# Kernel optimization log

Hardware: AMD Instinct MI355X
Metric: run time of the kernel (lower is better)

Reference implementation:

```python
import jax, jax.numpy as jnp
import numpy as np


def _gelu(x):
    # tf.nn.gelu default is exact (erf) gelu
    return jax.nn.gelu(x, approximate=False)


def _reduce_gat(x, W, A):
    # x: [..., n, f]; W: [f, d]; A: [2d, 1]
    wx = x @ W                                   # [..., n, d]
    root = jnp.broadcast_to(wx[..., 0:1, :], wx.shape)  # gather idx 0 + repeat
    cat = jnp.concatenate([wx, root], axis=-1)   # [..., n, 2d]
    z = _gelu(cat @ A)                           # Dense(1, activation=gelu)
    att = jax.nn.softmax(_gelu(z), axis=-2)      # gelu applied twice, then softmax over n
    return _gelu(jnp.sum(wx * att, axis=-2))     # [..., d]


def _layer(x, W, A):
    # W: [H, f, d], A: [H, 2d, 1]; mean over heads
    heads = jax.vmap(lambda w, a: _reduce_gat(x, w, a))(W, A)
    return jnp.mean(heads, axis=0)


def setup_inputs() -> dict:
    key = jax.random.key(0)
    k = jax.random.split(key, 5)
    B, N2, N1, F, D, H = 512, 16, 16, 256, 256, 4
    x = jax.random.normal(k[0], (B, N2, N1, F), dtype=jnp.float32)
    W0 = jax.random.normal(k[1], (H, F, D), dtype=jnp.float32) * 0.05
    A0 = jax.random.normal(k[2], (H, 2 * D, 1), dtype=jnp.float32) * 0.05
    W1 = jax.random.normal(k[3], (H, D, D), dtype=jnp.float32) * 0.05
    A1 = jax.random.normal(k[4], (H, 2 * D, 1), dtype=jnp.float32) * 0.05
    return {"x": x, "W0": W0, "A0": A0, "W1": W1, "A1": A1}


def reference(x, W0, A0, W1, A1):
    x = _layer(x, W0, A0)  # [B, N2, D]
    x = _layer(x, W1, A1)  # [B, D]
    return x
```

## Files before the change

kernel.cpp:

```cpp
#include <hip/hip_runtime.h>
#include <math.h>

typedef _Float16 half_t;
typedef __attribute__((ext_vector_type(8))) _Float16 half8;
typedef __attribute__((ext_vector_type(16))) float floatx16;

__device__ __forceinline__ float gelu_exact(float v) {
    return 0.5f * v * (1.0f + erff(v * 0.7071067811865476f));
}

__device__ __forceinline__ floatx16 zero16() {
    floatx16 z;
#pragma unroll
    for (int i = 0; i < 16; ++i) z[i] = 0.f;
    return z;
}

#define MFMA16(a, b, c) __builtin_amdgcn_mfma_f32_32x32x16_f16((a), (b), (c), 0, 0, 0)

__global__ __launch_bounds__(256) void prep(const float* __restrict__ W0,
                                            const float* __restrict__ A0,
                                            const float* __restrict__ W1,
                                            const float* __restrict__ A1,
                                            half_t* __restrict__ Wsw0, half_t* __restrict__ Wsw1,
                                            half_t* __restrict__ Zah0, half_t* __restrict__ Zal0,
                                            half_t* __restrict__ Zah1, half_t* __restrict__ Zal1) {
    __shared__ float tile[32][257];
    const int t  = threadIdx.x;
    const int kb = blockIdx.x & 7;
    const int h  = (blockIdx.x >> 3) & 3;
    const int tz = blockIdx.x >> 5;
    const float* W = tz ? W1 : W0;
    const float* A = tz ? A1 : A0;
    half_t* Wsw = tz ? Wsw1 : Wsw0;
    half_t* Zh  = tz ? Zah1 : Zah0;
    half_t* Zl  = tz ? Zal1 : Zal0;

    for (int i = 0; i < 32; ++i)
        tile[i][t] = W[(size_t)(h * 256 + kb * 32 + i) * 256 + t];
    __syncthreads();

    const int j = t >> 5, lmn = t & 31;
#pragma unroll
    for (int i0 = 0; i0 < 32; i0 += 8) {
        const int ks = 2 * kb + (i0 >> 4);
        const int q  = (i0 >> 3) & 1;
        half_t hb[8];
#pragma unroll
        for (int ii = 0; ii < 8; ++ii) hb[ii] = (half_t)tile[i0 + ii][t];
        size_t off = ((size_t)(h * 16 + ks) * 8 + j) * 512 + (size_t)(32 * q + lmn) * 8;
        *(half8*)&Wsw[off] = *(half8*)hb;
    }

    if (kb == 0) {
        const float4* Wr = (const float4*)&W[(size_t)(h * 256 + t) * 256];
        const float4* Al = (const float4*)&A[h * 512];
        const float4* Ah = (const float4*)&A[h * 512 + 256];
        float wl = 0.f, wh = 0.f;
        for (int d = 0; d < 64; ++d) {
            float4 wv = Wr[d], a0 = Al[d], a1 = Ah[d];
            wl += wv.x * a0.x + wv.y * a0.y + wv.z * a0.z + wv.w * a0.w;
            wh += wv.x * a1.x + wv.y * a1.y + wv.z * a1.z + wv.w * a1.w;
        }
        half_t hi = (half_t)wl;
        Zh[(2 * h) * 256 + t] = hi;
        Zl[(2 * h) * 256 + t] = (half_t)(wl - (float)hi);
        hi = (half_t)wh;
        Zh[(2 * h + 1) * 256 + t] = hi;
        Zl[(2 * h + 1) * 256 + t] = (half_t)(wh - (float)hi);
        if (h == 0) {
            for (int c = 8; c < 32; ++c) {
                Zh[c * 256 + t] = (half_t)0.f;
                Zl[c * 256 + t] = (half_t)0.f;
            }
        }
    }
}

template <int GROUPS>
__global__ __launch_bounds__(256, 2) void gat_layer(
    const float* __restrict__ x,
    const half_t* __restrict__ Wsw,
    const half_t* __restrict__ Zah, const half_t* __restrict__ Zal,
    float* __restrict__ out) {
    constexpr int ROWS = GROUPS * 16;
    constexpr int MT   = ROWS / 32;

    __shared__ half_t xsh[MT * 16 * 512];
    __shared__ half_t xsl[MT * 16 * 512];
    __shared__ float zlo_s[4][ROWS];
    __shared__ float zhi_s[4][ROWS];
    __shared__ float ge_s[4][ROWS];
    __shared__ float att_s[4][ROWS];

    const int t  = threadIdx.x;
    const int w  = t >> 6;
    const int l  = t & 63;
    const int lm = t & 31;
    const int q  = (t >> 5) & 1;

    {
        const float4* xg = (const float4*)(x + (size_t)blockIdx.x * ROWS * 256);
#pragma unroll
        for (int i = 0; i < ROWS / 8; ++i) {
            int e = t + 256 * i;
            int row = e >> 5, cc = e & 31;
            float4 v0 = xg[row * 64 + 2 * cc];
            float4 v1 = xg[row * 64 + 2 * cc + 1];
            half_t hb[8], lb[8];
            const float* vf = &v0.x;
#pragma unroll
            for (int ii = 0; ii < 8; ++ii) {
                float v = (ii < 4) ? vf[ii] : (&v1.x)[ii - 4];
                half_t hv = (half_t)v;
                hb[ii] = hv;
                lb[ii] = (half_t)(v - (float)hv);
            }
            int m = row >> 5, r31 = row & 31, ks = cc >> 1, kq = cc & 1;
            int base = ((m * 16 + ks) * 64 + 32 * kq + r31) * 8;
            *(half8*)&xsh[base] = *(half8*)hb;
            *(half8*)&xsl[base] = *(half8*)lb;
        }
    }
    __syncthreads();

    if (w == 0) {
        floatx16 zm[MT], zc[MT];
#pragma unroll
        for (int mt = 0; mt < MT; ++mt) { zm[mt] = zero16(); zc[mt] = zero16(); }
#pragma unroll 4
        for (int ks = 0; ks < 16; ++ks) {
            const int ko = lm * 256 + 16 * ks + 8 * q;
            half8 bh = *(const half8*)&Zah[ko];
            half8 bl = *(const half8*)&Zal[ko];
#pragma unroll
            for (int mt = 0; mt < MT; ++mt) {
                half8 a  = *(const half8*)&xsh[((mt * 16 + ks) * 64 + l) * 8];
                half8 al = *(const half8*)&xsl[((mt * 16 + ks) * 64 + l) * 8];
                zm[mt] = MFMA16(a, bh, zm[mt]);
                zc[mt] = MFMA16(al, bh, zc[mt]);
                zc[mt] = MFMA16(a, bl, zc[mt]);
            }
        }
        if (lm < 8) {
            int h = lm >> 1;
            float* dst = (lm & 1) ? &zhi_s[h][0] : &zlo_s[h][0];
#pragma unroll
            for (int mt = 0; mt < MT; ++mt)
#pragma unroll
                for (int r = 0; r < 16; ++r) {
                    int row = 32 * mt + 4 * q + (r & 3) + 8 * (r >> 2);
                    dst[row] = zm[mt][r] + zc[mt][r];
                }
        }
    }
    __syncthreads();

    {
        int h = t >> 6, r = t & 63;
        if (r < ROWS) {
            float z = zlo_s[h][r] + zhi_s[h][r & ~15];
            ge_s[h][r] = gelu_exact(gelu_exact(z));
        }
    }
    __syncthreads();
    {
        int h = t >> 6, r = t & 63;
        if (r < ROWS) {
            int g0 = r & ~15;
            float mx = -1e30f;
#pragma unroll
            for (int i = 0; i < 16; ++i) mx = fmaxf(mx, ge_s[h][g0 + i]);
            float s = 0.f;
#pragma unroll
            for (int i = 0; i < 16; ++i) s += expf(ge_s[h][g0 + i] - mx);
            att_s[h][r] = expf(ge_s[h][r] - mx) / s;
        }
    }
    __syncthreads();

    float outp[2][GROUPS];
#pragma unroll
    for (int nt = 0; nt < 2; ++nt)
#pragma unroll
        for (int g = 0; g < GROUPS; ++g) outp[nt][g] = 0.f;

#pragma unroll 1
    for (int h = 0; h < 4; ++h) {
        float tp[2][GROUPS];
#pragma unroll
        for (int nt = 0; nt < 2; ++nt)
#pragma unroll
            for (int g = 0; g < GROUPS; ++g) tp[nt][g] = 0.f;

        const half_t* Bp = Wsw + ((size_t)(h * 16) * 8 + 2 * w) * 512 + (size_t)l * 8;

#pragma unroll 1
        for (int pass = 0; pass < 2; ++pass) {
            const half_t* Xp = pass ? xsl : xsh;
            floatx16 acc[MT][2];
#pragma unroll
            for (int mt = 0; mt < MT; ++mt) { acc[mt][0] = zero16(); acc[mt][1] = zero16(); }

#pragma unroll
            for (int ks = 0; ks < 16; ++ks) {
                half8 b0 = *(const half8*)(Bp + (size_t)ks * 4096);
                half8 b1 = *(const half8*)(Bp + (size_t)ks * 4096 + 512);
#pragma unroll
                for (int mt = 0; mt < MT; ++mt) {
                    half8 a = *(const half8*)&Xp[((mt * 16 + ks) * 64 + l) * 8];
                    acc[mt][0] = MFMA16(a, b0, acc[mt][0]);
                    acc[mt][1] = MFMA16(a, b1, acc[mt][1]);
                }
            }

#pragma unroll
            for (int mt = 0; mt < MT; ++mt)
#pragma unroll
                for (int k = 0; k < 4; ++k) {
                    float4 a4 = *(const float4*)&att_s[h][32 * mt + 4 * q + 8 * k];
#pragma unroll
                    for (int jj = 0; jj < 4; ++jj) {
                        int r = 4 * k + jj;
                        int row = 32 * mt + 4 * q + 8 * k + jj;
                        int g = row >> 4;
                        float av = (&a4.x)[jj];
                        tp[0][g] = fmaf(acc[mt][0][r], av, tp[0][g]);
                        tp[1][g] = fmaf(acc[mt][1][r], av, tp[1][g]);
                    }
                }
        }

#pragma unroll
        for (int nt = 0; nt < 2; ++nt)
#pragma unroll
            for (int g = 0; g < GROUPS; ++g) {
                float s = tp[nt][g] + __shfl_xor(tp[nt][g], 32, 64);
                outp[nt][g] += gelu_exact(s);
            }
    }

    if (q == 0) {
#pragma unroll
        for (int g = 0; g < GROUPS; ++g) {
            size_t ro = ((size_t)blockIdx.x * GROUPS + g) * 256 + 64 * w;
            out[ro + lm]      = 0.25f * outp[0][g];
            out[ro + 32 + lm] = 0.25f * outp[1][g];
        }
    }
}

extern "C" void kernel_launch(void* const* d_in, const int* in_sizes, int n_in,
                              void* d_out, int out_size, void* d_ws, size_t ws_size,
                              hipStream_t stream) {
    const float* x  = (const float*)d_in[0];
    const float* W0 = (const float*)d_in[1];
    const float* A0 = (const float*)d_in[2];
    const float* W1 = (const float*)d_in[3];
    const float* A1 = (const float*)d_in[4];

    char* ws = (char*)d_ws;
    float*  y1   = (float*)ws;
    half_t* Wsw0 = (half_t*)(ws + 8388608);
    half_t* Wsw1 = (half_t*)(ws + 8912896);
    half_t* Zah0 = (half_t*)(ws + 9437184);
    half_t* Zal0 = (half_t*)(ws + 9453568);
    half_t* Zah1 = (half_t*)(ws + 9469952);
    half_t* Zal1 = (half_t*)(ws + 9486336);

    prep<<<64, 256, 0, stream>>>(W0, A0, W1, A1, Wsw0, Wsw1, Zah0, Zal0, Zah1, Zal1);
    gat_layer<4><<<2048, 256, 0, stream>>>(x, Wsw0, Zah0, Zal0, y1);
    gat_layer<2><<<256, 256, 0, stream>>>(y1, Wsw1, Zah1, Zal1, (float*)d_out);
}
```

Measured before the change: 347.8 us.

## Split GAT layers into smaller blocks, swizzle LDS, spread z-phase across waves

Layer 1 now uses 32-row blocks (4096 blocks, occupancy hint 4) instead of 64-row blocks. The z-projection is split across all four waves by K-slices and reduced through shared memory, where before only wave 0 did it. Layer 2 uses 1024-thread blocks that give each wave one head/strip pair in parallel and reduce the heads through LDS. The shared-memory A tiles get an XOR swizzle to avoid bank conflicts, and the hi/lo MFMA passes are merged into one accumulator. The trade-offs are more blocks that each re-read the weights, plus extra synchronisation.

New measurement: 480.6 us. 38.2% more time.

```diff
diff --git a/kernel.cpp b/kernel.cpp
--- a/kernel.cpp
+++ b/kernel.cpp
@@ -15,6 +15,8 @@
     for (int i = 0; i < 16; ++i) z[i] = 0.f;
     return z;
 }
+
+__device__ __forceinline__ int swz(int b) { return b ^ (((b >> 9) & 7) << 4); }
 
 #define MFMA16(a, b, c) __builtin_amdgcn_mfma_f32_32x32x16_f16((a), (b), (c), 0, 0, 0)
 
@@ -44,11 +46,11 @@
 #pragma unroll
     for (int i0 = 0; i0 < 32; i0 += 8) {
         const int ks = 2 * kb + (i0 >> 4);
-        const int q  = (i0 >> 3) & 1;
+        const int qq = (i0 >> 3) & 1;
         half_t hb[8];
 #pragma unroll
         for (int ii = 0; ii < 8; ++ii) hb[ii] = (half_t)tile[i0 + ii][t];
-        size_t off = ((size_t)(h * 16 + ks) * 8 + j) * 512 + (size_t)(32 * q + lmn) * 8;
+        size_t off = ((size_t)(h * 16 + ks) * 8 + j) * 512 + (size_t)(32 * qq + lmn) * 8;
         *(half8*)&Wsw[off] = *(half8*)hb;
     }
 
@@ -77,164 +79,144 @@
     }
 }
 
-template <int GROUPS>
-__global__ __launch_bounds__(256, 2) void gat_layer(
-    const float* __restrict__ x,
-    const half_t* __restrict__ Wsw,
+
+__device__ __forceinline__ void stage_chunk(const float4* __restrict__ xg,
+                                            half_t* __restrict__ xsh,
+                                            half_t* __restrict__ xsl, int e) {
+    int row = e >> 5, cc = e & 31;
+    float4 v0 = xg[row * 64 + 2 * cc];
+    float4 v1 = xg[row * 64 + 2 * cc + 1];
+    half_t hb[8], lb[8];
+#pragma unroll
+    for (int ii = 0; ii < 8; ++ii) {
+        float v = (ii < 4) ? (&v0.x)[ii] : (&v1.x)[ii - 4];
+        half_t hv = (half_t)v;
+        hb[ii] = hv;
+        lb[ii] = (half_t)(v - (float)hv);
+    }
+    int base = ((cc >> 1) * 64 + 32 * (cc & 1) + row) * 16;
+    *(half8*)((char*)xsh + swz(base)) = *(half8*)hb;
+    *(half8*)((char*)xsl + swz(base)) = *(half8*)lb;
+}
+
+__device__ __forceinline__ void z_phase(const half_t* __restrict__ xsh,
+                                        const half_t* __restrict__ xsl,
+                                        const half_t* __restrict__ Zah,
+                                        const half_t* __restrict__ Zal,
+                                        float* __restrict__ zrow,
+                                        int w, int l, int lm, int q) {
+    floatx16 zp = zero16();
+#pragma unroll
+    for (int kk = 0; kk < 4; ++kk) {
+        int ks = 4 * w + kk;
+        int ko = lm * 256 + 16 * ks + 8 * q;
+        half8 bh = *(const half8*)&Zah[ko];
+        half8 bl = *(const half8*)&Zal[ko];
+        int ao = (ks * 64 + l) * 16;
+        half8 ah = *(const half8*)((const char*)xsh + swz(ao));
+        half8 al = *(const half8*)((const char*)xsl + swz(ao));
+        zp = MFMA16(ah, bh, zp);
+        zp = MFMA16(al, bh, zp);
+        zp = MFMA16(ah, bl, zp);
+    }
+    if (lm < 8) {
+#pragma unroll
+        for (int r = 0; r < 16; ++r) {
+            int row = 4 * q + (r & 3) + 8 * (r >> 2);
+            zrow[row * 9 + lm] = zp[r];
+        }
+    }
+}
+
+__device__ __forceinline__ void head_gemm(const half_t* __restrict__ xsh,
+                                          const half_t* __restrict__ xsl,
+                                          const half_t* __restrict__ Bp,
+                                          const float* __restrict__ att_h,
+                                          int l, int q, float tp[2][2]) {
+    floatx16 acc0 = zero16(), acc1 = zero16();
+#pragma unroll
+    for (int ks = 0; ks < 16; ++ks) {
+        half8 b0 = *(const half8*)(Bp + (size_t)ks * 4096);
+        half8 b1 = *(const half8*)(Bp + (size_t)ks * 4096 + 512);
+        int ao = (ks * 64 + l) * 16;
+        half8 ah = *(const half8*)((const char*)xsh + swz(ao));
+        half8 al = *(const half8*)((const char*)xsl + swz(ao));
+        acc0 = MFMA16(ah, b0, acc0);
+        acc0 = MFMA16(al, b0, acc0);
+        acc1 = MFMA16(ah, b1, acc1);
+        acc1 = MFMA16(al, b1, acc1);
+    }
+    tp[0][0] = tp[0][1] = tp[1][0] = tp[1][1] = 0.f;
+#pragma unroll
+    for (int k = 0; k < 4; ++k) {
+        float4 a4 = *(const float4*)&att_h[4 * q + 8 * k];
+        int g = k >> 1;
+#pragma unroll
+        for (int jj = 0; jj < 4; ++jj) {
+            int r = 4 * k + jj;
+            float av = (&a4.x)[jj];
+            tp[0][g] = fmaf(acc0[r], av, tp[0][g]);
+            tp[1][g] = fmaf(acc1[r], av, tp[1][g]);
+        }
+    }
+}
+
+__global__ __launch_bounds__(256, 4) void gat1(
+    const float* __restrict__ x, const half_t* __restrict__ Wsw,
     const half_t* __restrict__ Zah, const half_t* __restrict__ Zal,
     float* __restrict__ out) {
-    constexpr int ROWS = GROUPS * 16;
-    constexpr int MT   = ROWS / 32;
-
-    __shared__ half_t xsh[MT * 16 * 512];
-    __shared__ half_t xsl[MT * 16 * 512];
-    __shared__ float zlo_s[4][ROWS];
-    __shared__ float zhi_s[4][ROWS];
-    __shared__ float ge_s[4][ROWS];
-    __shared__ float att_s[4][ROWS];
-
-    const int t  = threadIdx.x;
-    const int w  = t >> 6;
-    const int l  = t & 63;
-    const int lm = t & 31;
-    const int q  = (t >> 5) & 1;
-
-    {
-        const float4* xg = (const float4*)(x + (size_t)blockIdx.x * ROWS * 256);
-#pragma unroll
-        for (int i = 0; i < ROWS / 8; ++i) {
-            int e = t + 256 * i;
-            int row = e >> 5, cc = e & 31;
-            float4 v0 = xg[row * 64 + 2 * cc];
-            float4 v1 = xg[row * 64 + 2 * cc + 1];
-            half_t hb[8], lb[8];
-            const float* vf = &v0.x;
-#pragma unroll
-            for (int ii = 0; ii < 8; ++ii) {
-                float v = (ii < 4) ? vf[ii] : (&v1.x)[ii - 4];
-                half_t hv = (half_t)v;
-                hb[ii] = hv;
-                lb[ii] = (half_t)(v - (float)hv);
-            }
-            int m = row >> 5, r31 = row & 31, ks = cc >> 1, kq = cc & 1;
-            int base = ((m * 16 + ks) * 64 + 32 * kq + r31) * 8;
-            *(half8*)&xsh[base] = *(half8*)hb;
-            *(half8*)&xsl[base] = *(half8*)lb;
-        }
-    }
-    __syncthreads();
-
-    if (w == 0) {
-        floatx16 zm[MT], zc[MT];
-#pragma unroll
-        for (int mt = 0; mt < MT; ++mt) { zm[mt] = zero16(); zc[mt] = zero16(); }
-#pragma unroll 4
-        for (int ks = 0; ks < 16; ++ks) {
-            const int ko = lm * 256 + 16 * ks + 8 * q;
-            half8 bh = *(const half8*)&Zah[ko];
-            half8 bl = *(const half8*)&Zal[ko];
-#pragma unroll
-            for (int mt = 0; mt < MT; ++mt) {
-                half8 a  = *(const half8*)&xsh[((mt * 16 + ks) * 64 + l) * 8];
-                half8 al = *(const half8*)&xsl[((mt * 16 + ks) * 64 + l) * 8];
-                zm[mt] = MFMA16(a, bh, zm[mt]);
-                zc[mt] = MFMA16(al, bh, zc[mt]);
-                zc[mt] = MFMA16(a, bl, zc[mt]);
-            }
-        }
-        if (lm < 8) {
-            int h = lm >> 1;
-            float* dst = (lm & 1) ? &zhi_s[h][0] : &zlo_s[h][0];
-#pragma unroll
-            for (int mt = 0; mt < MT; ++mt)
-#pragma unroll
-                for (int r = 0; r < 16; ++r) {
-                    int row = 32 * mt + 4 * q + (r & 3) + 8 * (r >> 2);
-                    dst[row] = zm[mt][r] + zc[mt][r];
-                }
-        }
-    }
+    __shared__ __align__(16) half_t xsh[16 * 512];
+    __shared__ __align__(16) half_t xsl[16 * 512];
+    __shared__ float zpart[4][32][9];
+    __shared__ __align__(16) float ge_s[4][32];
+    __shared__ __align__(16) float att_s[4][32];
+
+    const int t = threadIdx.x;
+    const int w = t >> 6, l = t & 63, lm = t & 31, q = (t >> 5) & 1;
+
+    const float4* xg = (const float4*)(x + (size_t)blockIdx.x * 32 * 256);
+#pragma unroll
+    for (int i = 0; i < 4; ++i) stage_chunk(xg, xsh, xsl, t + 256 * i);
+    __syncthreads();
+
+    z_phase(xsh, xsl, Zah, Zal, &zpart[w][0][0], w, l, lm, q);
     __syncthreads();
 
     {
         int h = t >> 6, r = t & 63;
-        if (r < ROWS) {
-            float z = zlo_s[h][r] + zhi_s[h][r & ~15];
-            ge_s[h][r] = gelu_exact(gelu_exact(z));
+        if (r < 32) {
+            int c0 = 2 * h, c1 = 2 * h + 1, rr = r & ~15;
+            float own  = zpart[0][r][c0] + zpart[1][r][c0] + zpart[2][r][c0] + zpart[3][r][c0];
+            float root = zpart[0][rr][c1] + zpart[1][rr][c1] + zpart[2][rr][c1] + zpart[3][rr][c1];
+            ge_s[h][r] = gelu_exact(gelu_exact(own + root));
         }
     }
     __syncthreads();
     {
         int h = t >> 6, r = t & 63;
-        if (r < ROWS) {
+        if (r < 32) {
             int g0 = r & ~15;
             float mx = -1e30f;
 #pragma unroll
             for (int i = 0; i < 16; ++i) mx = fmaxf(mx, ge_s[h][g0 + i]);
-            float s = 0.f;
-#pragma unroll
-            for (int i = 0; i < 16; ++i) s += expf(ge_s[h][g0 + i] - mx);
-            att_s[h][r] = expf(ge_s[h][r] - mx) / s;
-        }
-    }
-    __syncthreads();
-
-    float outp[2][GROUPS];
-#pragma unroll
-    for (int nt = 0; nt < 2; ++nt)
-#pragma unroll
-        for (int g = 0; g < GROUPS; ++g) outp[nt][g] = 0.f;
-
+            float sum = 0.f;
+#pragma unroll
+            for (int i = 0; i < 16; ++i) sum += expf(ge_s[h][g0 + i] - mx);
+            att_s[h][r] = expf(ge_s[h][r] - mx) / sum;
+        }
+    }
+    __syncthreads();
+
+    float outp[2][2] = {{0.f, 0.f}, {0.f, 0.f}};
 #pragma unroll 1
     for (int h = 0; h < 4; ++h) {
-        float tp[2][GROUPS];
+        const half_t* Bp = Wsw + ((size_t)(h * 16) * 8 + 2 * w) * 512 + (size_t)l * 8;
+        float tp[2][2];
+        head_gemm(xsh, xsl, Bp, &att_s[h][0], l, q, tp);
 #pragma unroll
         for (int nt = 0; nt < 2; ++nt)
 #pragma unroll
-            for (int g = 0; g < GROUPS; ++g) tp[nt][g] = 0.f;
-
-        const half_t* Bp = Wsw + ((size_t)(h * 16) * 8 + 2 * w) * 512 + (size_t)l * 8;
-
-#pragma unroll 1
-        for (int pass = 0; pass < 2; ++pass) {
-            const half_t* Xp = pass ? xsl : xsh;
-            floatx16 acc[MT][2];
-#pragma unroll
-            for (int mt = 0; mt < MT; ++mt) { acc[mt][0] = zero16(); acc[mt][1] = zero16(); }
-
-#pragma unroll
-            for (int ks = 0; ks < 16; ++ks) {
-                half8 b0 = *(const half8*)(Bp + (size_t)ks * 4096);
-                half8 b1 = *(const half8*)(Bp + (size_t)ks * 4096 + 512);
-#pragma unroll
-                for (int mt = 0; mt < MT; ++mt) {
-                    half8 a = *(const half8*)&Xp[((mt * 16 + ks) * 64 + l) * 8];
-                    acc[mt][0] = MFMA16(a, b0, acc[mt][0]);
-                    acc[mt][1] = MFMA16(a, b1, acc[mt][1]);
-                }
-            }
-
-#pragma unroll
-            for (int mt = 0; mt < MT; ++mt)
-#pragma unroll
-                for (int k = 0; k < 4; ++k) {
-                    float4 a4 = *(const float4*)&att_s[h][32 * mt + 4 * q + 8 * k];
-#pragma unroll
-                    for (int jj = 0; jj < 4; ++jj) {
-                        int r = 4 * k + jj;
-                        int row = 32 * mt + 4 * q + 8 * k + jj;
-                        int g = row >> 4;
-                        float av = (&a4.x)[jj];
-                        tp[0][g] = fmaf(acc[mt][0][r], av, tp[0][g]);
-                        tp[1][g] = fmaf(acc[mt][1][r], av, tp[1][g]);
-                    }
-                }
-        }
-
-#pragma unroll
-        for (int nt = 0; nt < 2; ++nt)
-#pragma unroll
-            for (int g = 0; g < GROUPS; ++g) {
+            for (int g = 0; g < 2; ++g) {
                 float s = tp[nt][g] + __shfl_xor(tp[nt][g], 32, 64);
                 outp[nt][g] += gelu_exact(s);
             }
@@ -242,11 +224,73 @@
 
     if (q == 0) {
 #pragma unroll
-        for (int g = 0; g < GROUPS; ++g) {
-            size_t ro = ((size_t)blockIdx.x * GROUPS + g) * 256 + 64 * w;
+        for (int g = 0; g < 2; ++g) {
+            size_t ro = ((size_t)blockIdx.x * 2 + g) * 256 + 64 * w;
             out[ro + lm]      = 0.25f * outp[0][g];
             out[ro + 32 + lm] = 0.25f * outp[1][g];
         }
+    }
+}
+
+__global__ __launch_bounds__(1024, 1) void gat2(
+    const float* __restrict__ x, const half_t* __restrict__ Wsw,
+    const half_t* __restrict__ Zah, const half_t* __restrict__ Zal,
+    float* __restrict__ out) {
+    __shared__ __align__(16) half_t xsh[16 * 512];
+    __shared__ __align__(16) half_t xsl[16 * 512];
+    __shared__ float zpart[4][32][9];
+    __shared__ __align__(16) float ge_s[4][32];
+    __shared__ __align__(16) float att_s[4][32];
+    __shared__ float outp_s[4][2][256];
+
+    const int t = threadIdx.x;
+    const int w = t >> 6, l = t & 63, lm = t & 31, q = (t >> 5) & 1;
+
+    const float4* xg = (const float4*)(x + (size_t)blockIdx.x * 32 * 256);
+    stage_chunk(xg, xsh, xsl, t);
+    __syncthreads();
+
+    if (w < 4) z_phase(xsh, xsl, Zah, Zal, &zpart[w][0][0], w, l, lm, q);
+    __syncthreads();
+
+    if (t < 128) {
+        int h = t >> 5, r = t & 31;
+        int c0 = 2 * h, c1 = 2 * h + 1, rr = r & ~15;
+        float own  = zpart[0][r][c0] + zpart[1][r][c0] + zpart[2][r][c0] + zpart[3][r][c0];
+        float root = zpart[0][rr][c1] + zpart[1][rr][c1] + zpart[2][rr][c1] + zpart[3][rr][c1];
+        ge_s[h][r] = gelu_exact(gelu_exact(own + root));
+    }
+    __syncthreads();
+    if (t < 128) {
+        int h = t >> 5, r = t & 31;
+        int g0 = r & ~15;
+        float mx = -1e30f;
+#pragma unroll
+        for (int i = 0; i < 16; ++i) mx = fmaxf(mx, ge_s[h][g0 + i]);
+        float sum = 0.f;
+#pragma unroll
+        for (int i = 0; i < 16; ++i) sum += expf(ge_s[h][g0 + i] - mx);
+        att_s[h][r] = expf(ge_s[h][r] - mx) / sum;
+    }
+    __syncthreads();
+
+    const int head = w >> 2, strip = w & 3;
+    const half_t* Bp = Wsw + ((size_t)(head * 16) * 8 + 2 * strip) * 512 + (size_t)l * 8;
+    float tp[2][2];
+    head_gemm(xsh, xsl, Bp, &att_s[head][0], l, q, tp);
+#pragma unroll
+    for (int nt = 0; nt < 2; ++nt)
+#pragma unroll
+        for (int g = 0; g < 2; ++g) {
+            float s = tp[nt][g] + __shfl_xor(tp[nt][g], 32, 64);
+            if (q == 0) outp_s[head][g][64 * strip + 32 * nt + lm] = gelu_exact(s);
+        }
+    __syncthreads();
+
+    if (t < 512) {
+        int g = t >> 8, col = t & 255;
+        float s = outp_s[0][g][col] + outp_s[1][g][col] + outp_s[2][g][col] + outp_s[3][g][col];
+        out[((size_t)blockIdx.x * 2 + g) * 256 + col] = 0.25f * s;
     }
 }
 
@@ -269,6 +313,6 @@
     half_t* Zal1 = (half_t*)(ws + 9486336);
 
     prep<<<64, 256, 0, stream>>>(W0, A0, W1, A1, Wsw0, Wsw1, Zah0, Zal0, Zah1, Zal1);
-    gat_layer<4><<<2048, 256, 0, stream>>>(x, Wsw0, Zah0, Zal0, y1);
-    gat_layer<2><<<256, 256, 0, stream>>>(y1, Wsw1, Zah1, Zal1, (float*)d_out);
-}
+    gat1<<<4096, 256, 0, stream>>>(x, Wsw0, Zah0, Zal0, y1);
+    gat2<<<256, 1024, 0, stream>>>(y1, Wsw1, Zah1, Zal1, (float*)d_out);
+}
```

## Add dedicated second-layer GAT kernel with 512 threads and swizzled LDS

Applied to the files above, without the earlier changes.

Replaces the templated gat_layer<2> launch for the second layer with a new gat2 kernel that uses 512 threads per block. Each wave pair handles one head and half of the output columns, and the head outputs are reduced through shared memory. The staged input is split into fp16 hi/lo parts and stored in an XOR-swizzled LDS layout to avoid bank conflicts. The aim is more parallelism per block for the small 256-block second layer, which should shorten its latency, at the cost of extra sync points and shared-memory reductions.

After: 372.9 us. +7.2%, slower.

```diff
diff --git a/kernel.cpp b/kernel.cpp
--- a/kernel.cpp
+++ b/kernel.cpp
@@ -14,6 +14,14 @@
 #pragma unroll
     for (int i = 0; i < 16; ++i) z[i] = 0.f;
     return z;
+}
+
+__device__ __forceinline__ int swz(int b) { return b ^ (((b >> 9) & 7) << 4); }
+
+template <bool SWZ>
+__device__ __forceinline__ half8 lds_frag(const half_t* p, int byteoff) {
+    if (SWZ) byteoff = swz(byteoff);
+    return *(const half8*)((const char*)p + byteoff);
 }
 
 #define MFMA16(a, b, c) __builtin_amdgcn_mfma_f32_32x32x16_f16((a), (b), (c), 0, 0, 0)
@@ -44,11 +52,11 @@
 #pragma unroll
     for (int i0 = 0; i0 < 32; i0 += 8) {
         const int ks = 2 * kb + (i0 >> 4);
-        const int q  = (i0 >> 3) & 1;
+        const int qq = (i0 >> 3) & 1;
         half_t hb[8];
 #pragma unroll
         for (int ii = 0; ii < 8; ++ii) hb[ii] = (half_t)tile[i0 + ii][t];
-        size_t off = ((size_t)(h * 16 + ks) * 8 + j) * 512 + (size_t)(32 * q + lmn) * 8;
+        size_t off = ((size_t)(h * 16 + ks) * 8 + j) * 512 + (size_t)(32 * qq + lmn) * 8;
         *(half8*)&Wsw[off] = *(half8*)hb;
     }
 
@@ -250,6 +258,151 @@
     }
 }
 
+
+__device__ __forceinline__ void stage_chunk(const float4* __restrict__ xg,
+                                            half_t* __restrict__ xsh,
+                                            half_t* __restrict__ xsl, int e) {
+    int row = e >> 5, cc = e & 31;
+    float4 v0 = xg[row * 64 + 2 * cc];
+    float4 v1 = xg[row * 64 + 2 * cc + 1];
+    half_t hb[8], lb[8];
+#pragma unroll
+    for (int ii = 0; ii < 8; ++ii) {
+        float v = (ii < 4) ? (&v0.x)[ii] : (&v1.x)[ii - 4];
+        half_t hv = (half_t)v;
+        hb[ii] = hv;
+        lb[ii] = (half_t)(v - (float)hv);
+    }
+    int base = ((cc >> 1) * 64 + 32 * (cc & 1) + row) * 16;
+    *(half8*)((char*)xsh + swz(base)) = *(half8*)hb;
+    *(half8*)((char*)xsl + swz(base)) = *(half8*)lb;
+}
+
+__device__ __forceinline__ void z_phase(const half_t* __restrict__ xsh,
+                                        const half_t* __restrict__ xsl,
+                                        const half_t* __restrict__ Zah,
+                                        const half_t* __restrict__ Zal,
+                                        float* __restrict__ zrow,
+                                        int w, int l, int lm, int q) {
+    floatx16 zp = zero16();
+#pragma unroll
+    for (int kk = 0; kk < 4; ++kk) {
+        int ks = 4 * w + kk;
+        int ko = lm * 256 + 16 * ks + 8 * q;
+        half8 bh = *(const half8*)&Zah[ko];
+        half8 bl = *(const half8*)&Zal[ko];
+        int ao = (ks * 64 + l) * 16;
+        half8 ah = lds_frag<true>(xsh, ao);
+        half8 al = lds_frag<true>(xsl, ao);
+        zp = MFMA16(ah, bh, zp);
+        zp = MFMA16(al, bh, zp);
+        zp = MFMA16(ah, bl, zp);
+    }
+    if (lm < 8) {
+#pragma unroll
+        for (int r = 0; r < 16; ++r) {
+            int row = 4 * q + (r & 3) + 8 * (r >> 2);
+            zrow[row * 9 + lm] = zp[r];
+        }
+    }
+}
+
+__global__ __launch_bounds__(512, 1) void gat2(
+    const float* __restrict__ y1, const half_t* __restrict__ Wsw,
+    const half_t* __restrict__ Zah, const half_t* __restrict__ Zal,
+    float* __restrict__ out) {
+    __shared__ __align__(16) half_t xsh[16 * 512];
+    __shared__ __align__(16) half_t xsl[16 * 512];
+    __shared__ float zpart[4][32][9];
+    __shared__ __align__(16) float ge_s[4][32];
+    __shared__ __align__(16) float att_s[4][32];
+    __shared__ float outp_s[4][2][256];
+
+    const int t = threadIdx.x;
+    const int w = t >> 6, l = t & 63, lm = t & 31, q = (t >> 5) & 1;
+
+    const float4* xg = (const float4*)(y1 + (size_t)blockIdx.x * 32 * 256);
+    stage_chunk(xg, xsh, xsl, t);
+    stage_chunk(xg, xsh, xsl, t + 512);
+    __syncthreads();
+
+    if (w < 4) z_phase(xsh, xsl, Zah, Zal, &zpart[w][0][0], w, l, lm, q);
+    __syncthreads();
+
+    if (t < 128) {
+        int h = t >> 5, r = t & 31;
+        int c0 = 2 * h, c1 = 2 * h + 1, rr = r & ~15;
+        float own  = zpart[0][r][c0] + zpart[1][r][c0] + zpart[2][r][c0] + zpart[3][r][c0];
+        float root = zpart[0][rr][c1] + zpart[1][rr][c1] + zpart[2][rr][c1] + zpart[3][rr][c1];
+        ge_s[h][r] = gelu_exact(gelu_exact(own + root));
+    }
+    __syncthreads();
+    if (t < 128) {
+        int h = t >> 5, r = t & 31;
+        int g0 = r & ~15;
+        float mx = -1e30f;
+#pragma unroll
+        for (int i = 0; i < 16; ++i) mx = fmaxf(mx, ge_s[h][g0 + i]);
+        float sum = 0.f;
+#pragma unroll
+        for (int i = 0; i < 16; ++i) sum += expf(ge_s[h][g0 + i] - mx);
+        att_s[h][r] = expf(ge_s[h][r] - mx) / sum;
+    }
+    __syncthreads();
+
+    const int h = w >> 1, s = w & 1;
+    const half_t* Bp = Wsw + ((size_t)(h * 16) * 8 + 4 * s) * 512 + (size_t)l * 8;
+
+    float tp[4][2];
+#pragma unroll
+    for (int jc = 0; jc < 4; ++jc) { tp[jc][0] = 0.f; tp[jc][1] = 0.f; }
+
+#pragma unroll 1
+    for (int pass = 0; pass < 2; ++pass) {
+        const half_t* Xp = pass ? xsl : xsh;
+        floatx16 acc[4];
+#pragma unroll
+        for (int jc = 0; jc < 4; ++jc) acc[jc] = zero16();
+#pragma unroll
+        for (int ks = 0; ks < 16; ++ks) {
+            int ao = (ks * 64 + l) * 16;
+            half8 a = lds_frag<true>(Xp, ao);
+#pragma unroll
+            for (int jc = 0; jc < 4; ++jc) {
+                half8 b = *(const half8*)(Bp + (size_t)ks * 4096 + jc * 512);
+                acc[jc] = MFMA16(a, b, acc[jc]);
+            }
+        }
+#pragma unroll
+        for (int g = 0; g < 2; ++g)
+#pragma unroll
+            for (int k2 = 0; k2 < 2; ++k2)
+#pragma unroll
+                for (int jj = 0; jj < 4; ++jj) {
+                    float av = att_s[h][16 * g + 8 * k2 + 4 * q + jj];
+                    int r = jj + 4 * k2 + 8 * g;
+#pragma unroll
+                    for (int jc = 0; jc < 4; ++jc)
+                        tp[jc][g] = fmaf(acc[jc][r], av, tp[jc][g]);
+                }
+    }
+
+#pragma unroll
+    for (int g = 0; g < 2; ++g)
+#pragma unroll
+        for (int jc = 0; jc < 4; ++jc) {
+            float sf = tp[jc][g] + __shfl_xor(tp[jc][g], 32, 64);
+            if (q == 0) outp_s[h][g][128 * s + 32 * jc + lm] = gelu_exact(sf);
+        }
+    __syncthreads();
+
+    {
+        int g = t >> 8, col = t & 255;
+        float sm = outp_s[0][g][col] + outp_s[1][g][col] + outp_s[2][g][col] + outp_s[3][g][col];
+        out[((size_t)blockIdx.x * 2 + g) * 256 + col] = 0.25f * sm;
+    }
+}
+
 extern "C" void kernel_launch(void* const* d_in, const int* in_sizes, int n_in,
                               void* d_out, int out_size, void* d_ws, size_t ws_size,
                               hipStream_t stream) {
@@ -270,5 +423,5 @@
 
     prep<<<64, 256, 0, stream>>>(W0, A0, W1, A1, Wsw0, Wsw1, Zah0, Zal0, Zah1, Zal1);
     gat_layer<4><<<2048, 256, 0, stream>>>(x, Wsw0, Zah0, Zal0, y1);
-    gat_layer<2><<<256, 256, 0, stream>>>(y1, Wsw1, Zah1, Zal1, (float*)d_out);
-}
+    gat2<<<256, 512, 0, stream>>>(y1, Wsw1, Zah1, Zal1, (float*)d_out);
+}
```
